# Optimization experiments

Measured on AMD Instinct MI355X. Metric: run time of the kernel, lower is better.

Reference implementation:

```python
import jax, jax.numpy as jnp
import numpy as np

N_HEADS = 16
N_KV_HEADS = 4
HEAD_DIM = 128


def setup_inputs() -> dict:
    key = jax.random.key(0)
    ks = jax.random.split(key, 5)
    B, T, C = 4, 2048, 2048
    kv_dim = N_KV_HEADS * HEAD_DIM
    s = 0.02
    return {
        "x": jax.random.normal(ks[0], (B, T, C), jnp.float32),
        "Wq": jax.random.normal(ks[1], (C, C), jnp.float32) * s,
        "Wk": jax.random.normal(ks[2], (kv_dim, C), jnp.float32) * s,
        "Wv": jax.random.normal(ks[3], (kv_dim, C), jnp.float32) * s,
        "Wo": jax.random.normal(ks[4], (C, C), jnp.float32) * s,
    }


def reference(x, Wq, Wk, Wv, Wo):
    B, T, C = x.shape
    n_rep = N_HEADS // N_KV_HEADS
    # projections (nn.Linear: y = x @ W^T), reshape to (B, H, T, D)
    q = (x @ Wq.T).reshape(B, T, N_HEADS, HEAD_DIM).transpose(0, 2, 1, 3)
    k = (x @ Wk.T).reshape(B, T, N_KV_HEADS, HEAD_DIM).transpose(0, 2, 1, 3)
    v = (x @ Wv.T).reshape(B, T, N_KV_HEADS, HEAD_DIM).transpose(0, 2, 1, 3)
    # GQA: expand kv heads (repeat_interleave on head dim)
    k = jnp.repeat(k, n_rep, axis=1)
    v = jnp.repeat(v, n_rep, axis=1)
    scale = 1.0 / np.sqrt(HEAD_DIM).astype(np.float32)
    scores = jnp.einsum("bhqd,bhkd->bhqk", q, k) * scale
    causal = jnp.tril(jnp.ones((T, T), bool))
    scores = jnp.where(causal[None, None], scores, -jnp.inf)
    attn = jax.nn.softmax(scores, axis=-1)  # dropout p=0 -> identity
    out = jnp.einsum("bhqk,bhkd->bhqd", attn, v)
    out = out.transpose(0, 2, 1, 3).reshape(B, T, C)
    return out @ Wo.T
```

## Files before the change

kernel.cpp:

```cpp
#include <hip/hip_runtime.h>

#define TB 4
#define TT 2048
#define TC 2048
#define NH 16
#define NKV 4
#define HD 128
#define KVDIM (NKV*HD)
#define NQKV (TC + 2*KVDIM)
#define MTOK (TB*TT)

typedef __bf16 bf16x8 __attribute__((ext_vector_type(8)));
typedef __bf16 bf16x2 __attribute__((ext_vector_type(2)));
typedef float  f32x4  __attribute__((ext_vector_type(4)));
typedef float  f32x16 __attribute__((ext_vector_type(16)));
typedef unsigned short ushort_t;
typedef unsigned short us8 __attribute__((ext_vector_type(8)));
typedef unsigned short us4 __attribute__((ext_vector_type(4)));
typedef unsigned int u32x4 __attribute__((ext_vector_type(4)));
typedef unsigned int u32x2 __attribute__((ext_vector_type(2)));

#define QSC 0.12751743f

__device__ __forceinline__ ushort_t f2bf(float f) {
    unsigned u = __builtin_bit_cast(unsigned, f);
    u += 0x7fffu + ((u >> 16) & 1u);
    return (ushort_t)(u >> 16);
}

__device__ __forceinline__ unsigned pkbf(float lo, float hi) {
    bf16x2 v;
    v[0] = (__bf16)lo; v[1] = (__bf16)hi;
    return __builtin_bit_cast(unsigned, v);
}

__device__ __forceinline__ void gload16(const ushort_t* g, ushort_t* l) {
    __builtin_amdgcn_global_load_lds(
        (const __attribute__((address_space(1))) unsigned int*)g,
        (__attribute__((address_space(3))) unsigned int*)l, 16, 0, 0);
}

__global__ __launch_bounds__(256) void cast_bf16(const float* __restrict__ in,
                                                 ushort_t* __restrict__ out, long n) {
    long i = (long)blockIdx.x * blockDim.x + threadIdx.x;
    long stride = (long)gridDim.x * blockDim.x;
    for (long e = i * 4; e < n; e += stride * 4) {
        float4 v = *reinterpret_cast<const float4*>(in + e);
        us4 o;
        o[0] = f2bf(v.x); o[1] = f2bf(v.y); o[2] = f2bf(v.z); o[3] = f2bf(v.w);
        *reinterpret_cast<us4*>(out + e) = o;
    }
}

#define LBLK 8192

template<bool OUTF32, bool QSCALE>
__global__ __launch_bounds__(512, 2) void gemm256(const ushort_t* __restrict__ A,
                                                  const ushort_t* __restrict__ Bw,
                                                  float* __restrict__ Cf,
                                                  ushort_t* __restrict__ Cb,
                                                  int M, int N, int Kd, int nbn) {
    extern __shared__ ushort_t lds[];
    const int tid = threadIdx.x;
    const int lane = tid & 63, wid = tid >> 6;
    const int wm = wid >> 2, wn = wid & 3;
    const int g = lane >> 4, l16 = lane & 15;

    const int cpx = gridDim.x >> 3;
    const int swz = (blockIdx.x & 7) * cpx + (blockIdx.x >> 3);
    const int bm = swz / nbn, bn = swz % nbn;

    const ushort_t* Ag = A  + (size_t)bm * 256 * Kd;
    const ushort_t* Bg = Bw + (size_t)bn * 256 * Kd;

    const int r0 = tid >> 3;
    const int p0 = (tid & 7) ^ (r0 & 7);
    const size_t so0 = (size_t)r0 * Kd + p0 * 8;
    const size_t so1 = so0 + (size_t)64 * Kd;
    const int ldsw0 = wid * 512;

    f32x4 acc[8][4] = {};
    bf16x8 aA[4][2], bB[2][2];

    const int NK = Kd >> 6;
    const int NI = Kd >> 7;

#define STAGE(mat, half, tile) do { if ((tile) < NK) {                                   \
    const ushort_t* sg_ = ((mat) ? Bg : Ag) + (size_t)(half) * 128 * Kd + (size_t)(tile) * 64; \
    ushort_t* lb_ = lds + (((((tile)&1)*2 + (mat))*2 + (half)) * LBLK) + ldsw0;          \
    gload16(sg_ + so0, lb_);                                                             \
    gload16(sg_ + so1, lb_ + 4096);                                                      \
} } while(0)

#define LDA(buf, qm) do {                                                                \
    const ushort_t* Ah_ = lds + (((buf)*2 + 0)*2 + wm) * LBLK;                           \
    _Pragma("unroll") for (int mi_ = 0; mi_ < 4; mi_++) {                                \
        const int r_ = (qm)*64 + mi_*16 + l16;                                           \
        _Pragma("unroll") for (int ks_ = 0; ks_ < 2; ks_++)                              \
            aA[mi_][ks_] = *reinterpret_cast<const bf16x8*>(                             \
                Ah_ + r_*64 + (((ks_*4 + g) ^ (r_ & 7)) * 8));                           \
    }                                                                                    \
} while(0)

#define LDB(buf, qn) do {                                                                \
    const ushort_t* Bh_ = lds + (((buf)*2 + 1)*2 + (wn >> 1)) * LBLK;                    \
    _Pragma("unroll") for (int nj_ = 0; nj_ < 2; nj_++) {                                \
        const int r_ = (wn & 1)*64 + (qn)*32 + nj_*16 + l16;                             \
        _Pragma("unroll") for (int ks_ = 0; ks_ < 2; ks_++)                              \
            bB[nj_][ks_] = *reinterpret_cast<const bf16x8*>(                             \
                Bh_ + r_*64 + (((ks_*4 + g) ^ (r_ & 7)) * 8));                           \
    }                                                                                    \
} while(0)

#define MM(qm, qn) do {                                                                  \
    __builtin_amdgcn_s_setprio(1);                                                       \
    _Pragma("unroll") for (int mi_ = 0; mi_ < 4; mi_++)                                  \
    _Pragma("unroll") for (int nj_ = 0; nj_ < 2; nj_++)                                  \
    _Pragma("unroll") for (int ks_ = 0; ks_ < 2; ks_++)                                  \
        acc[(qm)*4 + mi_][(qn)*2 + nj_] = __builtin_amdgcn_mfma_f32_16x16x32_bf16(       \
            aA[mi_][ks_], bB[nj_][ks_], acc[(qm)*4 + mi_][(qn)*2 + nj_], 0, 0, 0);       \
    __builtin_amdgcn_s_setprio(0);                                                       \
} while(0)

#define PH_MID() do {                                                                    \
    __builtin_amdgcn_s_barrier();                                                        \
    asm volatile("s_waitcnt lgkmcnt(0)" ::: "memory");                                   \
    __builtin_amdgcn_sched_barrier(0);                                                   \
} while(0)

#define PH_END() __builtin_amdgcn_s_barrier()
#define PH_END_VM4() do { asm volatile("s_waitcnt vmcnt(4)" ::: "memory");               \
                          __builtin_amdgcn_s_barrier(); } while(0)
#define PH_END_VM0() do { asm volatile("s_waitcnt vmcnt(0)" ::: "memory");               \
                          __builtin_amdgcn_s_barrier(); } while(0)

    STAGE(0, 0, 0); STAGE(0, 1, 0); STAGE(1, 0, 0); STAGE(1, 1, 0);
    STAGE(0, 0, 1); STAGE(0, 1, 1);
    asm volatile("s_waitcnt vmcnt(4)" ::: "memory");
    __builtin_amdgcn_s_barrier();

    for (int i = 0; i < NI; ++i) {
        const int t0 = 2 * i, t1 = 2 * i + 1;
        const bool last = (i == NI - 1);
        LDA(0, 0); LDB(0, 0);
        STAGE(1, 0, t1); STAGE(1, 1, t1);
        PH_MID(); MM(0, 0); PH_END();
        LDB(0, 1);
        PH_MID(); MM(0, 1); PH_END();
        LDA(0, 1); LDB(0, 0);
        PH_MID(); MM(1, 0); PH_END();
        LDB(0, 1);
        STAGE(0, 0, t0 + 2); STAGE(0, 1, t0 + 2);
        PH_MID(); MM(1, 1);
        if (last) PH_END_VM0(); else PH_END_VM4();
        LDA(1, 0); LDB(1, 0);
        STAGE(1, 0, t0 + 2); STAGE(1, 1, t0 + 2);
        PH_MID(); MM(0, 0); PH_END();
        LDB(1, 1);
        PH_MID(); MM(0, 1); PH_END();
        LDA(1, 1); LDB(1, 0);
        PH_MID(); MM(1, 0); PH_END();
        LDB(1, 1);
        STAGE(0, 0, t1 + 2); STAGE(0, 1, t1 + 2);
        PH_MID(); MM(1, 1);
        if (last) PH_END_VM0(); else PH_END_VM4();
    }

#pragma unroll
    for (int mi = 0; mi < 8; mi++)
#pragma unroll
        for (int nj = 0; nj < 4; nj++) {
            const int rbase = bm * 256 + wm * 128 + mi * 16 + g * 4;
            const int col   = bn * 256 + wn * 64 + nj * 16 + l16;
#pragma unroll
            for (int r = 0; r < 4; r++) {
                float v = acc[mi][nj][r];
                if (QSCALE && col < TC) v *= QSC;
                size_t off = (size_t)(rbase + r) * N + col;
                if (OUTF32) Cf[off] = v;
                else        Cb[off] = __builtin_bit_cast(ushort_t, (__bf16)v);
            }
        }
#undef STAGE
#undef LDA
#undef LDB
#undef MM
#undef PH_MID
#undef PH_END
#undef PH_END_VM4
#undef PH_END_VM0
}

#define AQB 128
#define AKB 64
#define NTB (TT/AQB)
#define VTS 72

__global__ __launch_bounds__(256, 2) void attn_kernel(const ushort_t* __restrict__ qkv,
                                                      ushort_t* __restrict__ aout) {
    __shared__ alignas(16) ushort_t Ks[2][AKB * HD];
    __shared__ alignas(16) ushort_t Vt[2][HD * VTS];

    const int tid  = threadIdx.x;
    const int lane = tid & 63, wid = tid >> 6;
    const int hi   = lane >> 5, l31 = lane & 31;
    const int gx   = blockIdx.x;
    const int h    = blockIdx.y;
    const int b    = blockIdx.z;
    const int hk   = h >> 2;
    const size_t rowbase = (size_t)b * TT;

    const ushort_t* kg = qkv + TC + hk * HD;
    const ushort_t* vg = qkv + TC + KVDIM + hk * HD;
    const int rswz = (l31 & 7) << 3;

    us8 sk0, sk1, sk2, sk3;
    unsigned vv2[16];
    const int kr = tid >> 2, dcK = (tid & 3) * 32;
    const int vs = ((lane >> 2) & 7) << 3;

    for (int phase = 0; phase < 2; ++phase) {
        const int qb = (phase == 0 ? (NTB - 1 - gx) : gx) * AQB;
        const int q0 = qb + wid * 32;
        const int qrow = q0 + l31;

        bf16x8 qfr[8];
        {
            const ushort_t* qp = qkv + (rowbase + qrow) * NQKV + h * HD + hi * 8;
#pragma unroll
            for (int s = 0; s < 8; s++)
                qfr[s] = *reinterpret_cast<const bf16x8*>(qp + s * 16);
        }

        f32x16 oacc[4];
#pragma unroll
        for (int d = 0; d < 4; d++)
#pragma unroll
            for (int r = 0; r < 16; r++) oacc[d][r] = 0.f;
        float lsum = 0.f;

        const int ntiles = qb / AKB + 2;

        {
            const ushort_t* ksrc = kg + (rowbase + kr) * NQKV + dcK;
            sk0 = *reinterpret_cast<const us8*>(ksrc);
            sk1 = *reinterpret_cast<const us8*>(ksrc + 8);
            sk2 = *reinterpret_cast<const us8*>(ksrc + 16);
            sk3 = *reinterpret_cast<const us8*>(ksrc + 24);
            const ushort_t* vsrc = vg + (rowbase + wid * 16) * NQKV + 2 * lane;
#pragma unroll
            for (int j = 0; j < 16; j++)
                vv2[j] = *reinterpret_cast<const unsigned*>(vsrc + (size_t)j * NQKV);
        }
        if (phase) __syncthreads();

        for (int t = 0; t < ntiles; ++t) {
            const int kp0 = t * AKB;
            const int cur = t & 1;
            {
                const int kb = kr * HD + dcK, ksw = (kr & 7) << 3;
                *reinterpret_cast<us8*>(&Ks[cur][(kb     ) ^ ksw]) = sk0;
                *reinterpret_cast<us8*>(&Ks[cur][(kb +  8) ^ ksw]) = sk1;
                *reinterpret_cast<us8*>(&Ks[cur][(kb + 16) ^ ksw]) = sk2;
                *reinterpret_cast<us8*>(&Ks[cur][(kb + 24) ^ ksw]) = sk3;
                u32x4 pl0, ph0, pl1, ph1;
#pragma unroll
                for (int k = 0; k < 4; k++) {
                    pl0[k] = __builtin_amdgcn_perm(vv2[2 * k + 1], vv2[2 * k], 0x05040100u);
                    ph0[k] = __builtin_amdgcn_perm(vv2[2 * k + 1], vv2[2 * k], 0x07060302u);
                    pl1[k] = __builtin_amdgcn_perm(vv2[8 + 2 * k + 1], vv2[8 + 2 * k], 0x05040100u);
                    ph1[k] = __builtin_amdgcn_perm(vv2[8 + 2 * k + 1], vv2[8 + 2 * k], 0x07060302u);
                }
                ushort_t* r0 = &Vt[cur][(2 * lane) * VTS];
                ushort_t* r1 = &Vt[cur][(2 * lane + 1) * VTS];
                const int o0 = (wid * 16) ^ vs, o1 = (wid * 16 + 8) ^ vs;
                *reinterpret_cast<u32x4*>(r0 + o0) = pl0;
                *reinterpret_cast<u32x4*>(r0 + o1) = pl1;
                *reinterpret_cast<u32x4*>(r1 + o0) = ph0;
                *reinterpret_cast<u32x4*>(r1 + o1) = ph1;
            }
            if (t + 1 < ntiles) {
                const int kn = (t + 1) * AKB;
                const ushort_t* ksrc = kg + (rowbase + kn + kr) * NQKV + dcK;
                sk0 = *reinterpret_cast<const us8*>(ksrc);
                sk1 = *reinterpret_cast<const us8*>(ksrc + 8);
                sk2 = *reinterpret_cast<const us8*>(ksrc + 16);
                sk3 = *reinterpret_cast<const us8*>(ksrc + 24);
                const ushort_t* vsrc = vg + (rowbase + kn + wid * 16) * NQKV + 2 * lane;
#pragma unroll
                for (int j = 0; j < 16; j++)
                    vv2[j] = *reinterpret_cast<const unsigned*>(vsrc + (size_t)j * NQKV);
            }
            __syncthreads();

            if (kp0 <= q0 + 31) {
                f32x16 s0, s1;
#pragma unroll
                for (int r = 0; r < 16; r++) { s0[r] = 0.f; s1[r] = 0.f; }
                __builtin_amdgcn_s_setprio(1);
#pragma unroll
                for (int ds = 0; ds < 8; ds++) {
                    bf16x8 ka = *reinterpret_cast<const bf16x8*>(
                        &Ks[cur][(l31 * HD + ds * 16 + hi * 8) ^ rswz]);
                    s0 = __builtin_amdgcn_mfma_f32_32x32x16_bf16(ka, qfr[ds], s0, 0, 0, 0);
                }
#pragma unroll
                for (int ds = 0; ds < 8; ds++) {
                    bf16x8 ka = *reinterpret_cast<const bf16x8*>(
                        &Ks[cur][((32 + l31) * HD + ds * 16 + hi * 8) ^ rswz]);
                    s1 = __builtin_amdgcn_mfma_f32_32x32x16_bf16(ka, qfr[ds], s1, 0, 0, 0);
                }
                __builtin_amdgcn_s_setprio(0);
                if (kp0 + 63 > q0) {
#pragma unroll
                    for (int r = 0; r < 16; r++) {
                        int k0i = kp0 + (r & 3) + 8 * (r >> 2) + 4 * hi;
                        if (k0i > qrow)      s0[r] = -1e30f;
                        if (k0i + 32 > qrow) s1[r] = -1e30f;
                    }
                }
                unsigned pk0[8], pk1[8];
                float ps = 0.f;
#pragma unroll
                for (int w = 0; w < 8; w++) {
                    float a0 = exp2f(s0[2 * w]), a1 = exp2f(s0[2 * w + 1]);
                    float b0 = exp2f(s1[2 * w]), b1 = exp2f(s1[2 * w + 1]);
                    ps += (a0 + a1) + (b0 + b1);
                    pk0[w] = pkbf(a0, a1);
                    pk1[w] = pkbf(b0, b1);
                }
                ps += __shfl_xor(ps, 32);
                lsum += ps;
                __builtin_amdgcn_s_setprio(1);
#pragma unroll
                for (int ks = 0; ks < 4; ks++) {
                    const unsigned* pkt = (ks < 2) ? pk0 : pk1;
                    unsigned c00 = pkt[4 * (ks & 1) + 0];
                    unsigned c01 = pkt[4 * (ks & 1) + 1];
                    unsigned c10 = pkt[4 * (ks & 1) + 2];
                    unsigned c11 = pkt[4 * (ks & 1) + 3];
                    u32x2 rA = __builtin_amdgcn_permlane32_swap(c00, c10, false, false);
                    u32x2 rB = __builtin_amdgcn_permlane32_swap(c01, c11, false, false);
                    u32x4 faw;
                    faw[0] = rA[0];
                    faw[1] = rB[0];
                    faw[2] = rA[1];
                    faw[3] = rB[1];
                    bf16x8 pa = __builtin_bit_cast(bf16x8, faw);
#pragma unroll
                    for (int dt = 0; dt < 4; dt++) {
                        int doff = dt * 32 + l31;
                        int sr = ((doff >> 3) & 7) << 3;
                        bf16x8 vb = *reinterpret_cast<const bf16x8*>(
                            &Vt[cur][doff * VTS + ((ks * 16 + hi * 8) ^ sr)]);
                        oacc[dt] = __builtin_amdgcn_mfma_f32_32x32x16_bf16(vb, pa, oacc[dt], 0, 0, 0);
                    }
                }
                __builtin_amdgcn_s_setprio(0);
            }
        }

        const float rl = 1.f / lsum;
        ushort_t* orow = aout + (rowbase + qrow) * TC + h * HD;
#pragma unroll
        for (int dt = 0; dt < 4; dt++)
#pragma unroll
            for (int rp = 0; rp < 8; rp++) {
                int d = dt * 32 + ((2 * rp) & 3) + 8 * ((2 * rp) >> 2) + 4 * hi;
                unsigned w = pkbf(oacc[dt][2 * rp] * rl, oacc[dt][2 * rp + 1] * rl);
                *reinterpret_cast<unsigned*>(orow + d) = w;
            }
    }
}

extern "C" void kernel_launch(void* const* d_in, const int* in_sizes, int n_in,
                              void* d_out, int out_size, void* d_ws, size_t ws_size,
                              hipStream_t stream) {
    const float* x  = (const float*)d_in[0];
    const float* Wq = (const float*)d_in[1];
    const float* Wk = (const float*)d_in[2];
    const float* Wv = (const float*)d_in[3];
    const float* Wo = (const float*)d_in[4];
    float* out = (float*)d_out;

    ushort_t* x_bf  = (ushort_t*)d_ws;
    ushort_t* wqkv  = x_bf  + (size_t)MTOK * TC;
    ushort_t* wo_bf = wqkv  + (size_t)NQKV * TC;
    ushort_t* qkv   = wo_bf + (size_t)TC * TC;
    ushort_t* attn  = x_bf;

    auto nb = [](long n) { long b = (n / 4 + 255) / 256; return (int)(b > 4096 ? 4096 : b); };

    cast_bf16<<<nb((long)MTOK * TC), 256, 0, stream>>>(x, x_bf, (long)MTOK * TC);
    cast_bf16<<<nb((long)TC * TC),   256, 0, stream>>>(Wq, wqkv, (long)TC * TC);
    cast_bf16<<<nb((long)KVDIM * TC),256, 0, stream>>>(Wk, wqkv + (size_t)TC * TC, (long)KVDIM * TC);
    cast_bf16<<<nb((long)KVDIM * TC),256, 0, stream>>>(Wv, wqkv + (size_t)(TC + KVDIM) * TC, (long)KVDIM * TC);
    cast_bf16<<<nb((long)TC * TC),   256, 0, stream>>>(Wo, wo_bf, (long)TC * TC);

    const int GEMM_LDS = 131072;
    hipFuncSetAttribute(reinterpret_cast<const void*>(gemm256<false, true>),
                        hipFuncAttributeMaxDynamicSharedMemorySize, GEMM_LDS);
    hipFuncSetAttribute(reinterpret_cast<const void*>(gemm256<true, false>),
                        hipFuncAttributeMaxDynamicSharedMemorySize, GEMM_LDS);

    gemm256<false, true><<<dim3(384), 512, GEMM_LDS, stream>>>(
        x_bf, wqkv, nullptr, qkv, MTOK, NQKV, TC, NQKV / 256);

    attn_kernel<<<dim3(NTB / 2, NH, TB), 256, 0, stream>>>(qkv, attn);

    gemm256<true, false><<<dim3(256), 512, GEMM_LDS, stream>>>(
        attn, wo_bf, out, nullptr, MTOK, TC, TC, TC / 256);
}
```

Before: 324.4 us.

## Use triple-buffered 128x256 GEMM for QKV projection and fuse weight casts

Replaces the 256x256-tile QKV projection GEMM with a new 128x256-tile kernel using three LDS stages and twice as many blocks. This reduces wave-quantization tail imbalance across CUs and deepens the prefetch pipeline. The four separate weight cast launches are merged into one kernel writing a contiguous buffer. Smaller tiles lower per-block data reuse and raise LDS use per block.

Measured after the change: 326.2 us. No clear change (+0.6%).

```diff
diff --git a/kernel.cpp b/kernel.cpp
--- a/kernel.cpp
+++ b/kernel.cpp
@@ -49,6 +49,30 @@
         us4 o;
         o[0] = f2bf(v.x); o[1] = f2bf(v.y); o[2] = f2bf(v.z); o[3] = f2bf(v.w);
         *reinterpret_cast<us4*>(out + e) = o;
+    }
+}
+
+__global__ __launch_bounds__(256) void cast_w(const float* __restrict__ Wq,
+                                              const float* __restrict__ Wk,
+                                              const float* __restrict__ Wv,
+                                              const float* __restrict__ Wo,
+                                              ushort_t* __restrict__ dst) {
+    const long B1 = (long)TC * TC;
+    const long B2 = (long)(TC + KVDIM) * TC;
+    const long B3 = (long)NQKV * TC;
+    const long NW = B3 + (long)TC * TC;
+    long i = (long)blockIdx.x * blockDim.x + threadIdx.x;
+    long stride = (long)gridDim.x * blockDim.x;
+    for (long e = i * 4; e < NW; e += stride * 4) {
+        const float* src; long off;
+        if (e < B1)      { src = Wq; off = e; }
+        else if (e < B2) { src = Wk; off = e - B1; }
+        else if (e < B3) { src = Wv; off = e - B2; }
+        else             { src = Wo; off = e - B3; }
+        float4 v = *reinterpret_cast<const float4*>(src + off);
+        us4 o;
+        o[0] = f2bf(v.x); o[1] = f2bf(v.y); o[2] = f2bf(v.z); o[3] = f2bf(v.w);
+        *reinterpret_cast<us4*>(dst + e) = o;
     }
 }
 
@@ -191,6 +215,117 @@
 #undef PH_END_VM0
 }
 
+__global__ __launch_bounds__(512, 2) void gemm128(const ushort_t* __restrict__ A,
+                                                  const ushort_t* __restrict__ Bw,
+                                                  ushort_t* __restrict__ Cb,
+                                                  int N, int Kd, int nbn) {
+    extern __shared__ ushort_t lds[];
+    const int tid = threadIdx.x;
+    const int lane = tid & 63, wid = tid >> 6;
+    const int wm = wid >> 2, wn = wid & 3;
+    const int g = lane >> 4, l16 = lane & 15;
+
+    const int cpx = gridDim.x >> 3;
+    const int swz = (blockIdx.x & 7) * cpx + (blockIdx.x >> 3);
+    const int bm = swz / nbn, bn = swz % nbn;
+
+    const ushort_t* Ag = A  + (size_t)bm * 128 * Kd;
+    const ushort_t* Bg = Bw + (size_t)bn * 256 * Kd;
+
+    const int r0 = tid >> 3;
+    const int p0 = (tid & 7) ^ (r0 & 7);
+    const size_t so0 = (size_t)r0 * Kd + p0 * 8;
+    const size_t so1 = so0 + (size_t)64 * Kd;
+    const int ldsw0 = wid * 512;
+
+    f32x4 acc[4][4] = {};
+    bf16x8 aA[2][2], bB[4][2];
+    const int NK = Kd >> 6;
+
+#define STG(tile, bb_) do { if ((tile) < NK) {                                           \
+    const ushort_t* a_ = Ag + (size_t)(tile) * 64;                                       \
+    const ushort_t* b_ = Bg + (size_t)(tile) * 64;                                       \
+    gload16(a_ + so0, lds + ((bb_)*3 + 0) * 8192 + ldsw0);                               \
+    gload16(a_ + so1, lds + ((bb_)*3 + 0) * 8192 + ldsw0 + 4096);                        \
+    gload16(b_ + so0, lds + ((bb_)*3 + 1) * 8192 + ldsw0);                               \
+    gload16(b_ + so1, lds + ((bb_)*3 + 1) * 8192 + ldsw0 + 4096);                        \
+    gload16(b_ + (size_t)128 * Kd + so0, lds + ((bb_)*3 + 2) * 8192 + ldsw0);            \
+    gload16(b_ + (size_t)128 * Kd + so1, lds + ((bb_)*3 + 2) * 8192 + ldsw0 + 4096);     \
+} } while(0)
+
+#define LDA1(bb, qm) do {                                                                \
+    const ushort_t* Ah_ = lds + ((bb)*3 + 0) * 8192;                                     \
+    _Pragma("unroll") for (int mi_ = 0; mi_ < 2; mi_++) {                                \
+        const int r_ = wm*64 + (qm)*32 + mi_*16 + l16;                                   \
+        _Pragma("unroll") for (int ks_ = 0; ks_ < 2; ks_++)                              \
+            aA[mi_][ks_] = *reinterpret_cast<const bf16x8*>(                             \
+                Ah_ + r_*64 + (((ks_*4 + g) ^ (r_ & 7)) * 8));                           \
+    }                                                                                    \
+} while(0)
+
+#define LDB1(bb) do {                                                                    \
+    const ushort_t* Bh_ = lds + ((bb)*3 + 1 + (wn >> 1)) * 8192;                         \
+    _Pragma("unroll") for (int nj_ = 0; nj_ < 4; nj_++) {                                \
+        const int r_ = (wn & 1)*64 + nj_*16 + l16;                                       \
+        _Pragma("unroll") for (int ks_ = 0; ks_ < 2; ks_++)                              \
+            bB[nj_][ks_] = *reinterpret_cast<const bf16x8*>(                             \
+                Bh_ + r_*64 + (((ks_*4 + g) ^ (r_ & 7)) * 8));                           \
+    }                                                                                    \
+} while(0)
+
+#define MM1(qm) do {                                                                     \
+    __builtin_amdgcn_s_setprio(1);                                                       \
+    _Pragma("unroll") for (int mi_ = 0; mi_ < 2; mi_++)                                  \
+    _Pragma("unroll") for (int nj_ = 0; nj_ < 4; nj_++)                                  \
+    _Pragma("unroll") for (int ks_ = 0; ks_ < 2; ks_++)                                  \
+        acc[(qm)*2 + mi_][nj_] = __builtin_amdgcn_mfma_f32_16x16x32_bf16(                \
+            aA[mi_][ks_], bB[nj_][ks_], acc[(qm)*2 + mi_][nj_], 0, 0, 0);                \
+    __builtin_amdgcn_s_setprio(0);                                                       \
+} while(0)
+
+    STG(0, 0); STG(1, 1);
+    asm volatile("s_waitcnt vmcnt(6)" ::: "memory");
+    __builtin_amdgcn_s_barrier();
+
+    int cb = 0;
+    for (int t = 0; t < NK; ++t) {
+        const int sb = (cb == 0) ? 2 : cb - 1;
+        LDA1(cb, 0); LDB1(cb);
+        STG(t + 2, sb);
+        __builtin_amdgcn_s_barrier();
+        asm volatile("s_waitcnt lgkmcnt(0)" ::: "memory");
+        __builtin_amdgcn_sched_barrier(0);
+        MM1(0);
+        __builtin_amdgcn_s_barrier();
+        LDA1(cb, 1); LDB1(cb);
+        __builtin_amdgcn_s_barrier();
+        asm volatile("s_waitcnt lgkmcnt(0)" ::: "memory");
+        __builtin_amdgcn_sched_barrier(0);
+        MM1(1);
+        if (t + 2 < NK) asm volatile("s_waitcnt vmcnt(6)" ::: "memory");
+        else            asm volatile("s_waitcnt vmcnt(0)" ::: "memory");
+        __builtin_amdgcn_s_barrier();
+        cb = (cb == 2) ? 0 : cb + 1;
+    }
+
+#pragma unroll
+    for (int mi = 0; mi < 4; mi++)
+#pragma unroll
+        for (int nj = 0; nj < 4; nj++) {
+            const int rbase = bm * 128 + wm * 64 + mi * 16 + g * 4;
+            const int col   = bn * 256 + wn * 64 + nj * 16 + l16;
+            const float sc  = (col < TC) ? QSC : 1.f;
+#pragma unroll
+            for (int r = 0; r < 4; r++)
+                Cb[(size_t)(rbase + r) * N + col] =
+                    __builtin_bit_cast(ushort_t, (__bf16)(acc[mi][nj][r] * sc));
+        }
+#undef STG
+#undef LDA1
+#undef LDB1
+#undef MM1
+}
+
 #define AQB 128
 #define AKB 64
 #define NTB (TT/AQB)
@@ -271,13 +406,13 @@
                     pl1[k] = __builtin_amdgcn_perm(vv2[8 + 2 * k + 1], vv2[8 + 2 * k], 0x05040100u);
                     ph1[k] = __builtin_amdgcn_perm(vv2[8 + 2 * k + 1], vv2[8 + 2 * k], 0x07060302u);
                 }
-                ushort_t* r0 = &Vt[cur][(2 * lane) * VTS];
-                ushort_t* r1 = &Vt[cur][(2 * lane + 1) * VTS];
+                ushort_t* r0p = &Vt[cur][(2 * lane) * VTS];
+                ushort_t* r1p = &Vt[cur][(2 * lane + 1) * VTS];
                 const int o0 = (wid * 16) ^ vs, o1 = (wid * 16 + 8) ^ vs;
-                *reinterpret_cast<u32x4*>(r0 + o0) = pl0;
-                *reinterpret_cast<u32x4*>(r0 + o1) = pl1;
-                *reinterpret_cast<u32x4*>(r1 + o0) = ph0;
-                *reinterpret_cast<u32x4*>(r1 + o1) = ph1;
+                *reinterpret_cast<u32x4*>(r0p + o0) = pl0;
+                *reinterpret_cast<u32x4*>(r0p + o1) = pl1;
+                *reinterpret_cast<u32x4*>(r1p + o0) = ph0;
+                *reinterpret_cast<u32x4*>(r1p + o1) = ph1;
             }
             if (t + 1 < ntiles) {
                 const int kn = (t + 1) * AKB;
@@ -392,22 +527,19 @@
     auto nb = [](long n) { long b = (n / 4 + 255) / 256; return (int)(b > 4096 ? 4096 : b); };
 
     cast_bf16<<<nb((long)MTOK * TC), 256, 0, stream>>>(x, x_bf, (long)MTOK * TC);
-    cast_bf16<<<nb((long)TC * TC),   256, 0, stream>>>(Wq, wqkv, (long)TC * TC);
-    cast_bf16<<<nb((long)KVDIM * TC),256, 0, stream>>>(Wk, wqkv + (size_t)TC * TC, (long)KVDIM * TC);
-    cast_bf16<<<nb((long)KVDIM * TC),256, 0, stream>>>(Wv, wqkv + (size_t)(TC + KVDIM) * TC, (long)KVDIM * TC);
-    cast_bf16<<<nb((long)TC * TC),   256, 0, stream>>>(Wo, wo_bf, (long)TC * TC);
-
-    const int GEMM_LDS = 131072;
-    hipFuncSetAttribute(reinterpret_cast<const void*>(gemm256<false, true>),
-                        hipFuncAttributeMaxDynamicSharedMemorySize, GEMM_LDS);
+    cast_w<<<nb((long)NQKV * TC + (long)TC * TC), 256, 0, stream>>>(Wq, Wk, Wv, Wo, wqkv);
+
+    const int G128_LDS = 147456;
+    const int G256_LDS = 131072;
+    hipFuncSetAttribute(reinterpret_cast<const void*>(gemm128),
+                        hipFuncAttributeMaxDynamicSharedMemorySize, G128_LDS);
     hipFuncSetAttribute(reinterpret_cast<const void*>(gemm256<true, false>),
-                        hipFuncAttributeMaxDynamicSharedMemorySize, GEMM_LDS);
-
-    gemm256<false, true><<<dim3(384), 512, GEMM_LDS, stream>>>(
-        x_bf, wqkv, nullptr, qkv, MTOK, NQKV, TC, NQKV / 256);
+                        hipFuncAttributeMaxDynamicSharedMemorySize, G256_LDS);
+
+    gemm128<<<dim3(768), 512, G128_LDS, stream>>>(x_bf, wqkv, qkv, NQKV, TC, 12);
 
     attn_kernel<<<dim3(NTB / 2, NH, TB), 256, 0, stream>>>(qkv, attn);
 
-    gemm256<true, false><<<dim3(256), 512, GEMM_LDS, stream>>>(
+    gemm256<true, false><<<dim3(256), 512, G256_LDS, stream>>>(
         attn, wo_bf, out, nullptr, MTOK, TC, TC, TC / 256);
 }
```

## Replace 256x256 BK64 GEMM with 128x256 BK32 triple-buffered GEMM and fuse casts

Applied to the files above, without the earlier changes.

The GEMM is rewritten to use 128x256 output tiles with a K-step of 32 and a three-stage LDS ring, replacing the 256x256 double-buffered phase schedule. This doubles the grid, which should fill more CUs, and it simplifies synchronisation to one barrier per K-step. In exchange, each block gets less data reuse and pays more barriers per unit of work. The five separate fp32-to-bf16 cast launches are merged into one kernel writing a contiguous workspace, saving launch overhead.

New measurement: 326.4 us. About the same (+0.6%).

```diff
diff --git a/kernel.cpp b/kernel.cpp
--- a/kernel.cpp
+++ b/kernel.cpp
@@ -40,26 +40,39 @@
         (__attribute__((address_space(3))) unsigned int*)l, 16, 0, 0);
 }
 
-__global__ __launch_bounds__(256) void cast_bf16(const float* __restrict__ in,
-                                                 ushort_t* __restrict__ out, long n) {
+__global__ __launch_bounds__(256) void cast_all(const float* __restrict__ x,
+                                                const float* __restrict__ Wq,
+                                                const float* __restrict__ Wk,
+                                                const float* __restrict__ Wv,
+                                                const float* __restrict__ Wo,
+                                                ushort_t* __restrict__ dst) {
+    const long E0 = 16777216;
+    const long E1 = 20971520;
+    const long E2 = 22020096;
+    const long E3 = 23068672;
+    const long E4 = 27262976;
     long i = (long)blockIdx.x * blockDim.x + threadIdx.x;
     long stride = (long)gridDim.x * blockDim.x;
-    for (long e = i * 4; e < n; e += stride * 4) {
-        float4 v = *reinterpret_cast<const float4*>(in + e);
+    for (long e = i * 4; e < E4; e += stride * 4) {
+        const float* src; long off;
+        if (e < E0)      { src = x;  off = e; }
+        else if (e < E1) { src = Wq; off = e - E0; }
+        else if (e < E2) { src = Wk; off = e - E1; }
+        else if (e < E3) { src = Wv; off = e - E2; }
+        else             { src = Wo; off = e - E3; }
+        float4 v = *reinterpret_cast<const float4*>(src + off);
         us4 o;
         o[0] = f2bf(v.x); o[1] = f2bf(v.y); o[2] = f2bf(v.z); o[3] = f2bf(v.w);
-        *reinterpret_cast<us4*>(out + e) = o;
+        *reinterpret_cast<us4*>(dst + e) = o;
     }
 }
 
-#define LBLK 8192
-
 template<bool OUTF32, bool QSCALE>
-__global__ __launch_bounds__(512, 2) void gemm256(const ushort_t* __restrict__ A,
-                                                  const ushort_t* __restrict__ Bw,
-                                                  float* __restrict__ Cf,
-                                                  ushort_t* __restrict__ Cb,
-                                                  int M, int N, int Kd, int nbn) {
+__global__ __launch_bounds__(512, 2) void gemm_bk32(const ushort_t* __restrict__ A,
+                                                    const ushort_t* __restrict__ Bw,
+                                                    float* __restrict__ Cf,
+                                                    ushort_t* __restrict__ Cb,
+                                                    int N, int Kd, int nbn) {
     extern __shared__ ushort_t lds[];
     const int tid = threadIdx.x;
     const int lane = tid & 63, wid = tid >> 6;
@@ -70,107 +83,72 @@
     const int swz = (blockIdx.x & 7) * cpx + (blockIdx.x >> 3);
     const int bm = swz / nbn, bn = swz % nbn;
 
-    const ushort_t* Ag = A  + (size_t)bm * 256 * Kd;
+    const ushort_t* Ag = A  + (size_t)bm * 128 * Kd;
     const ushort_t* Bg = Bw + (size_t)bn * 256 * Kd;
 
-    const int r0 = tid >> 3;
-    const int p0 = (tid & 7) ^ (r0 & 7);
-    const size_t so0 = (size_t)r0 * Kd + p0 * 8;
-    const size_t so1 = so0 + (size_t)64 * Kd;
-    const int ldsw0 = wid * 512;
-
-    f32x4 acc[8][4] = {};
-    bf16x8 aA[4][2], bB[2][2];
-
-    const int NK = Kd >> 6;
-    const int NI = Kd >> 7;
-
-#define STAGE(mat, half, tile) do { if ((tile) < NK) {                                   \
-    const ushort_t* sg_ = ((mat) ? Bg : Ag) + (size_t)(half) * 128 * Kd + (size_t)(tile) * 64; \
-    ushort_t* lb_ = lds + (((((tile)&1)*2 + (mat))*2 + (half)) * LBLK) + ldsw0;          \
-    gload16(sg_ + so0, lb_);                                                             \
-    gload16(sg_ + so1, lb_ + 4096);                                                      \
+    const int arow = tid >> 2;
+    const int apos = (tid & 3) ^ (arow & 3);
+    const size_t aso  = (size_t)arow * Kd + apos * 8;
+    const size_t bso0 = aso;
+    const size_t bso1 = aso + (size_t)128 * Kd;
+    const int ldsw = wid * 512;
+
+    f32x4 acc[4][4] = {};
+    bf16x8 aA[4], bB[4];
+    const int NK = Kd >> 5;
+
+#define STG(tile, bb) do { if ((tile) < NK) {                                            \
+    const ushort_t* a_ = Ag + (size_t)(tile) * 32;                                       \
+    const ushort_t* b_ = Bg + (size_t)(tile) * 32;                                       \
+    ushort_t* lb_ = lds + (bb) * 12288 + ldsw;                                           \
+    gload16(a_ + aso,  lb_);                                                             \
+    gload16(b_ + bso0, lb_ + 4096);                                                      \
+    gload16(b_ + bso1, lb_ + 8192);                                                      \
 } } while(0)
 
-#define LDA(buf, qm) do {                                                                \
-    const ushort_t* Ah_ = lds + (((buf)*2 + 0)*2 + wm) * LBLK;                           \
+#define LDAB(bb) do {                                                                    \
+    const ushort_t* Ah_ = lds + (bb) * 12288;                                            \
+    const ushort_t* Bh_ = Ah_ + 4096;                                                    \
     _Pragma("unroll") for (int mi_ = 0; mi_ < 4; mi_++) {                                \
-        const int r_ = (qm)*64 + mi_*16 + l16;                                           \
-        _Pragma("unroll") for (int ks_ = 0; ks_ < 2; ks_++)                              \
-            aA[mi_][ks_] = *reinterpret_cast<const bf16x8*>(                             \
-                Ah_ + r_*64 + (((ks_*4 + g) ^ (r_ & 7)) * 8));                           \
+        const int r_ = wm * 64 + mi_ * 16 + l16;                                         \
+        aA[mi_] = *reinterpret_cast<const bf16x8*>(Ah_ + r_ * 32 + ((g ^ (r_ & 3)) * 8));\
+    }                                                                                    \
+    _Pragma("unroll") for (int nj_ = 0; nj_ < 4; nj_++) {                                \
+        const int r_ = wn * 64 + nj_ * 16 + l16;                                         \
+        bB[nj_] = *reinterpret_cast<const bf16x8*>(Bh_ + r_ * 32 + ((g ^ (r_ & 3)) * 8));\
     }                                                                                    \
 } while(0)
 
-#define LDB(buf, qn) do {                                                                \
-    const ushort_t* Bh_ = lds + (((buf)*2 + 1)*2 + (wn >> 1)) * LBLK;                    \
-    _Pragma("unroll") for (int nj_ = 0; nj_ < 2; nj_++) {                                \
-        const int r_ = (wn & 1)*64 + (qn)*32 + nj_*16 + l16;                             \
-        _Pragma("unroll") for (int ks_ = 0; ks_ < 2; ks_++)                              \
-            bB[nj_][ks_] = *reinterpret_cast<const bf16x8*>(                             \
-                Bh_ + r_*64 + (((ks_*4 + g) ^ (r_ & 7)) * 8));                           \
-    }                                                                                    \
-} while(0)
-
-#define MM(qm, qn) do {                                                                  \
-    __builtin_amdgcn_s_setprio(1);                                                       \
-    _Pragma("unroll") for (int mi_ = 0; mi_ < 4; mi_++)                                  \
-    _Pragma("unroll") for (int nj_ = 0; nj_ < 2; nj_++)                                  \
-    _Pragma("unroll") for (int ks_ = 0; ks_ < 2; ks_++)                                  \
-        acc[(qm)*4 + mi_][(qn)*2 + nj_] = __builtin_amdgcn_mfma_f32_16x16x32_bf16(       \
-            aA[mi_][ks_], bB[nj_][ks_], acc[(qm)*4 + mi_][(qn)*2 + nj_], 0, 0, 0);       \
-    __builtin_amdgcn_s_setprio(0);                                                       \
-} while(0)
-
-#define PH_MID() do {                                                                    \
-    __builtin_amdgcn_s_barrier();                                                        \
-    asm volatile("s_waitcnt lgkmcnt(0)" ::: "memory");                                   \
-    __builtin_amdgcn_sched_barrier(0);                                                   \
-} while(0)
-
-#define PH_END() __builtin_amdgcn_s_barrier()
-#define PH_END_VM4() do { asm volatile("s_waitcnt vmcnt(4)" ::: "memory");               \
-                          __builtin_amdgcn_s_barrier(); } while(0)
-#define PH_END_VM0() do { asm volatile("s_waitcnt vmcnt(0)" ::: "memory");               \
-                          __builtin_amdgcn_s_barrier(); } while(0)
-
-    STAGE(0, 0, 0); STAGE(0, 1, 0); STAGE(1, 0, 0); STAGE(1, 1, 0);
-    STAGE(0, 0, 1); STAGE(0, 1, 1);
-    asm volatile("s_waitcnt vmcnt(4)" ::: "memory");
+    STG(0, 0); STG(1, 1);
+    asm volatile("s_waitcnt vmcnt(3)" ::: "memory");
     __builtin_amdgcn_s_barrier();
 
-    for (int i = 0; i < NI; ++i) {
-        const int t0 = 2 * i, t1 = 2 * i + 1;
-        const bool last = (i == NI - 1);
-        LDA(0, 0); LDB(0, 0);
-        STAGE(1, 0, t1); STAGE(1, 1, t1);
-        PH_MID(); MM(0, 0); PH_END();
-        LDB(0, 1);
-        PH_MID(); MM(0, 1); PH_END();
-        LDA(0, 1); LDB(0, 0);
-        PH_MID(); MM(1, 0); PH_END();
-        LDB(0, 1);
-        STAGE(0, 0, t0 + 2); STAGE(0, 1, t0 + 2);
-        PH_MID(); MM(1, 1);
-        if (last) PH_END_VM0(); else PH_END_VM4();
-        LDA(1, 0); LDB(1, 0);
-        STAGE(1, 0, t0 + 2); STAGE(1, 1, t0 + 2);
-        PH_MID(); MM(0, 0); PH_END();
-        LDB(1, 1);
-        PH_MID(); MM(0, 1); PH_END();
-        LDA(1, 1); LDB(1, 0);
-        PH_MID(); MM(1, 0); PH_END();
-        LDB(1, 1);
-        STAGE(0, 0, t1 + 2); STAGE(0, 1, t1 + 2);
-        PH_MID(); MM(1, 1);
-        if (last) PH_END_VM0(); else PH_END_VM4();
+    int cb = 0;
+    for (int t = 0; t < NK; ++t) {
+        const int sb = (cb == 0) ? 2 : cb - 1;
+        STG(t + 2, sb);
+        LDAB(cb);
+        asm volatile("s_waitcnt lgkmcnt(0)" ::: "memory");
+        __builtin_amdgcn_sched_barrier(0);
+        __builtin_amdgcn_s_setprio(1);
+#pragma unroll
+        for (int mi = 0; mi < 4; mi++)
+#pragma unroll
+            for (int nj = 0; nj < 4; nj++)
+                acc[mi][nj] = __builtin_amdgcn_mfma_f32_16x16x32_bf16(
+                    aA[mi], bB[nj], acc[mi][nj], 0, 0, 0);
+        __builtin_amdgcn_s_setprio(0);
+        if (t + 2 < NK) asm volatile("s_waitcnt vmcnt(3)" ::: "memory");
+        else            asm volatile("s_waitcnt vmcnt(0)" ::: "memory");
+        __builtin_amdgcn_s_barrier();
+        cb = (cb == 2) ? 0 : cb + 1;
     }
 
 #pragma unroll
-    for (int mi = 0; mi < 8; mi++)
+    for (int mi = 0; mi < 4; mi++)
 #pragma unroll
         for (int nj = 0; nj < 4; nj++) {
-            const int rbase = bm * 256 + wm * 128 + mi * 16 + g * 4;
+            const int rbase = bm * 128 + wm * 64 + mi * 16 + g * 4;
             const int col   = bn * 256 + wn * 64 + nj * 16 + l16;
 #pragma unroll
             for (int r = 0; r < 4; r++) {
@@ -181,14 +159,8 @@
                 else        Cb[off] = __builtin_bit_cast(ushort_t, (__bf16)v);
             }
         }
-#undef STAGE
-#undef LDA
-#undef LDB
-#undef MM
-#undef PH_MID
-#undef PH_END
-#undef PH_END_VM4
-#undef PH_END_VM0
+#undef STG
+#undef LDAB
 }
 
 #define AQB 128
@@ -271,13 +243,13 @@
                     pl1[k] = __builtin_amdgcn_perm(vv2[8 + 2 * k + 1], vv2[8 + 2 * k], 0x05040100u);
                     ph1[k] = __builtin_amdgcn_perm(vv2[8 + 2 * k + 1], vv2[8 + 2 * k], 0x07060302u);
                 }
-                ushort_t* r0 = &Vt[cur][(2 * lane) * VTS];
-                ushort_t* r1 = &Vt[cur][(2 * lane + 1) * VTS];
+                ushort_t* r0p = &Vt[cur][(2 * lane) * VTS];
+                ushort_t* r1p = &Vt[cur][(2 * lane + 1) * VTS];
                 const int o0 = (wid * 16) ^ vs, o1 = (wid * 16 + 8) ^ vs;
-                *reinterpret_cast<u32x4*>(r0 + o0) = pl0;
-                *reinterpret_cast<u32x4*>(r0 + o1) = pl1;
-                *reinterpret_cast<u32x4*>(r1 + o0) = ph0;
-                *reinterpret_cast<u32x4*>(r1 + o1) = ph1;
+                *reinterpret_cast<u32x4*>(r0p + o0) = pl0;
+                *reinterpret_cast<u32x4*>(r0p + o1) = pl1;
+                *reinterpret_cast<u32x4*>(r1p + o0) = ph0;
+                *reinterpret_cast<u32x4*>(r1p + o1) = ph1;
             }
             if (t + 1 < ntiles) {
                 const int kn = (t + 1) * AKB;
@@ -389,25 +361,19 @@
     ushort_t* qkv   = wo_bf + (size_t)TC * TC;
     ushort_t* attn  = x_bf;
 
-    auto nb = [](long n) { long b = (n / 4 + 255) / 256; return (int)(b > 4096 ? 4096 : b); };
-
-    cast_bf16<<<nb((long)MTOK * TC), 256, 0, stream>>>(x, x_bf, (long)MTOK * TC);
-    cast_bf16<<<nb((long)TC * TC),   256, 0, stream>>>(Wq, wqkv, (long)TC * TC);
-    cast_bf16<<<nb((long)KVDIM * TC),256, 0, stream>>>(Wk, wqkv + (size_t)TC * TC, (long)KVDIM * TC);
-    cast_bf16<<<nb((long)KVDIM * TC),256, 0, stream>>>(Wv, wqkv + (size_t)(TC + KVDIM) * TC, (long)KVDIM * TC);
-    cast_bf16<<<nb((long)TC * TC),   256, 0, stream>>>(Wo, wo_bf, (long)TC * TC);
-
-    const int GEMM_LDS = 131072;
-    hipFuncSetAttribute(reinterpret_cast<const void*>(gemm256<false, true>),
-                        hipFuncAttributeMaxDynamicSharedMemorySize, GEMM_LDS);
-    hipFuncSetAttribute(reinterpret_cast<const void*>(gemm256<true, false>),
-                        hipFuncAttributeMaxDynamicSharedMemorySize, GEMM_LDS);
-
-    gemm256<false, true><<<dim3(384), 512, GEMM_LDS, stream>>>(
-        x_bf, wqkv, nullptr, qkv, MTOK, NQKV, TC, NQKV / 256);
+    cast_all<<<4096, 256, 0, stream>>>(x, Wq, Wk, Wv, Wo, x_bf);
+
+    const int G_LDS = 73728;
+    hipFuncSetAttribute(reinterpret_cast<const void*>(gemm_bk32<false, true>),
+                        hipFuncAttributeMaxDynamicSharedMemorySize, G_LDS);
+    hipFuncSetAttribute(reinterpret_cast<const void*>(gemm_bk32<true, false>),
+                        hipFuncAttributeMaxDynamicSharedMemorySize, G_LDS);
+
+    gemm_bk32<false, true><<<dim3(768), 512, G_LDS, stream>>>(
+        x_bf, wqkv, nullptr, qkv, NQKV, TC, 12);
 
     attn_kernel<<<dim3(NTB / 2, NH, TB), 256, 0, stream>>>(qkv, attn);
 
-    gemm256<true, false><<<dim3(256), 512, GEMM_LDS, stream>>>(
-        attn, wo_bf, out, nullptr, MTOK, TC, TC, TC / 256);
-}
+    gemm_bk32<true, false><<<dim3(512), 512, G_LDS, stream>>>(
+        attn, wo_bf, out, nullptr, TC, TC, 8);
+}
```
